# Kernel optimization log

Measured on AMD Instinct MI355X. Metric: run time of the kernel, lower is better.

Reference implementation:

```python
import jax, jax.numpy as jnp
import numpy as np

B, C, N, K, H = 8, 64, 4096, 32, 4
D = C // H  # head dim = 16
EPS = 1e-5  # BatchNorm eps (torch default)


def setup_inputs() -> dict:
    key = jax.random.key(0)
    ks = jax.random.split(key, 7)
    s = 0.05
    return {
        "x": jax.random.normal(ks[0], (B, C, N), jnp.float32),
        "wq": jax.random.normal(ks[1], (C, C), jnp.float32) * s,
        "wk": jax.random.normal(ks[2], (C, C), jnp.float32) * s,
        "wv": jax.random.normal(ks[3], (C, C), jnp.float32) * s,
        "w1": jax.random.normal(ks[4], (4 * C, C), jnp.float32) * s,
        "w2": jax.random.normal(ks[5], (C, 4 * C), jnp.float32) * s,
        "g1": jnp.ones((C,), jnp.float32),
        "b1": jnp.zeros((C,), jnp.float32),
        "g2": jnp.ones((C,), jnp.float32),
        "b2": jnp.zeros((C,), jnp.float32),
    }


def _bn(f, g, b):
    # BatchNorm1d in training mode: stats over (batch, points) per channel.
    # f: (B, N, C)
    mu = jnp.mean(f, axis=(0, 1))
    var = jnp.var(f, axis=(0, 1))  # biased, as torch uses for normalization
    return (f - mu) * jax.lax.rsqrt(var + EPS) * g + b


def reference(x, wq, wk, wv, w1, w2, g1, b1, g2, b2):
    feat = jnp.transpose(x, (0, 2, 1))  # (B, N, C)
    # KNN in feature space: negative squared distances, take top-K largest
    sq = jnp.sum(feat * feat, axis=-1)  # (B, N)
    neg_d = 2.0 * jnp.einsum('bnc,bmc->bnm', feat, feat) - sq[:, :, None] - sq[:, None, :]
    _, idx = jax.lax.top_k(neg_d, K)  # (B, N, K) int32
    # gather neighbors and form diffs
    nbrs = jax.vmap(lambda p, i: p[i])(feat, idx)  # (B, N, K, C)
    diff = nbrs - feat[:, :, None, :]
    # 1x1-conv projections (bias-free linear over channels)
    q = jnp.einsum('bnc,oc->bno', feat, wq).reshape(B, N, H, D)
    k = jnp.einsum('bnkc,oc->bnko', diff, wk).reshape(B, N, K, H, D)
    v = jnp.einsum('bnkc,oc->bnko', diff, wv).reshape(B, N, K, H, D)
    energy = jnp.einsum('bnhd,bnkhd->bnhk', q, k) / jnp.sqrt(jnp.float32(D))
    attn = jax.nn.softmax(energy, axis=-1)  # softmax over K neighbors
    out = jnp.einsum('bnhk,bnkhd->bnhd', attn, v).reshape(B, N, C)  # H-major merge
    f1 = _bn(feat + out, g1, b1)
    hid = jnp.einsum('bnc,oc->bno', f1, w1)
    hid = jnp.where(hid > 0, hid, 0.2 * hid)  # LeakyReLU(0.2)
    ff = jnp.einsum('bno,co->bnc', hid, w2)
    f2 = _bn(f1 + ff, g2, b2)
    return jnp.transpose(f2, (0, 2, 1))  # (B, C, N)
```

## Files before the change

### kernel.cpp

```cpp
#include <hip/hip_runtime.h>

#define Bdim 8
#define Cdim 64
#define Ndim 4096
#define Kdim 32
#define ROWS (Bdim*Ndim)
#define BN_EPS 1e-5f

using f32x4  = __attribute__((ext_vector_type(4))) float;
using f16x8  = __attribute__((ext_vector_type(8))) _Float16;

__device__ __forceinline__ float dot4(float4 a, float4 b){
  return a.x*b.x + a.y*b.y + a.z*b.z + a.w*b.w;
}
__device__ __forceinline__ int wofs(int o, int g){ return o*64 + (((g ^ ((o>>2)&7)))<<2); }
__device__ __forceinline__ unsigned keyOf(float f){
  unsigned u = __float_as_uint(f);
  return (u & 0x80000000u) ? ~u : (u ^ 0x80000000u);
}

__global__ __launch_bounds__(256) void prep_proj_kernel(const float* __restrict__ x,
    const float* __restrict__ wq, const float* __restrict__ wk,
    const float* __restrict__ wv,
    float* __restrict__ sq,
    float* __restrict__ Qo, float* __restrict__ PKo, float* __restrict__ PVo,
    float* __restrict__ accZ,
    float* __restrict__ featT, unsigned short* __restrict__ xh)
{
  __shared__ __align__(16) float ftile[64*68];
  __shared__ __align__(16) float Ws[3][64*64];
  const int tid = threadIdx.x;
  const int blk = blockIdx.x;
  const int b  = blk & 7;
  const int n0 = (blk >> 3) * 64;
  const size_t rowBase = (size_t)b*Ndim + n0;
  if (blk == 0) accZ[tid] = 0.f;
  for (int k=0;k<16;++k){
    int idx = tid + (k<<8);
    int c = idx>>6, nn = idx&63;
    ftile[nn*68+c] = x[((size_t)b*64+c)*Ndim + n0 + nn];
  }
  {
    const float* wp[3] = {wq, wk, wv};
    for (int m=0;m<3;++m)
      for (int k=0;k<16;++k){
        int idx = tid + (k<<8);
        int o = idx>>6, c = idx&63;
        Ws[m][wofs(o, c>>2) + (c&3)] = wp[m][o*64 + c];
      }
  }
  __syncthreads();
  for (int k=0;k<16;++k){
    int idx = tid + (k<<8);
    int r = idx>>6, c = idx&63;
    float v = ftile[r*68+c];
    size_t o = (rowBase + r)*64 + c;
    featT[o] = v;
    _Float16 hh = (_Float16)v;
    xh[o] = *reinterpret_cast<unsigned short*>(&hh);
  }
  if (tid < 64){
    float a = 0.f;
    #pragma unroll
    for (int c=0;c<64;++c){ float v = ftile[tid*68+c]; a += v*v; }
    sq[b*Ndim + n0 + tid] = a;
  }
  const int tr = tid>>4, to = tid&15;
  float* outp[3] = {Qo, PKo, PVo};
  for (int m=0;m<3;++m){
    float acc[4][4];
    #pragma unroll
    for (int r=0;r<4;++r){ acc[r][0]=0.f; acc[r][1]=0.f; acc[r][2]=0.f; acc[r][3]=0.f; }
    #pragma unroll 4
    for (int c4=0;c4<16;++c4){
      float4 f[4], w[4];
      #pragma unroll
      for (int r=0;r<4;++r)  f[r] = *(const float4*)&ftile[(4*tr+r)*68 + (c4<<2)];
      #pragma unroll
      for (int oo=0;oo<4;++oo) w[oo] = *(const float4*)&Ws[m][wofs(4*to+oo, c4)];
      #pragma unroll
      for (int r=0;r<4;++r)
        #pragma unroll
        for (int oo=0;oo<4;++oo)
          acc[r][oo] += dot4(f[r], w[oo]);
    }
    #pragma unroll
    for (int r=0;r<4;++r){
      float4 v; v.x=acc[r][0]; v.y=acc[r][1]; v.z=acc[r][2]; v.w=acc[r][3];
      *(float4*)&outp[m][(rowBase + 4*tr + r)*64 + 4*to] = v;
    }
  }
}

__global__ __launch_bounds__(1024) void knn_attn_kernel(
    const float* __restrict__ sq,
    const float* __restrict__ Qm, const float* __restrict__ PKm, const float* __restrict__ PVm,
    const float* __restrict__ featT, const unsigned short* __restrict__ xh,
    float* __restrict__ t1, float* __restrict__ bn1s, float* __restrict__ bn1q)
{
  __shared__ __align__(16) unsigned char smem[43328];
  float* fnS  = (float*)smem;
  float* qvS  = (float*)(smem + 4096);
  float* pknS = (float*)(smem + 8192);
  float* pvnS = (float*)(smem + 12288);
  unsigned short* dbuf = (unsigned short*)(smem + 16384);
  int*   candI  = (int*)(smem + 16384);
  float* red1   = (float*)(smem + 20480);
  float* red2   = (float*)(smem + 24576);
  float* enS    = (float*)(smem + 33024);
  int*   outIdx = (int*)(smem + 41216);
  float* sqnS   = (float*)(smem + 43264);

  const int tid  = threadIdx.x;
  const int lane = tid & 63;
  const int w    = tid >> 6;
  const int blk  = blockIdx.x;
  const int b    = blk & 7;
  const int n0   = (blk >> 3) << 4;
  const size_t b4096 = (size_t)b << 12;

  {
    int j = tid>>6, c = tid&63;
    size_t ro = (b4096 + n0 + j)*64 + c;
    fnS[tid]  = featT[ro];
    qvS[tid]  = Qm[ro];
    pknS[tid] = PKm[ro];
    pvnS[tid] = PVm[ro];
    if (tid < 16) sqnS[tid] = sq[b4096 + n0 + tid];
    if (tid < 512) outIdx[tid] = n0 + (tid>>5);
  }
  __syncthreads();

  const unsigned short* xhb = xh + (b4096 << 6);
  const float* sqb = sq + b4096;
  const int l15  = lane & 15;
  const int acol = (lane >> 4) << 3;
  const int qrow = (lane >> 4) << 2;

  unsigned kk[32];

  {
    f16x8 a0 = *(const f16x8*)&xhb[(size_t)(n0 + l15)*64 + acol];
    f16x8 a1 = *(const f16x8*)&xhb[(size_t)(n0 + l15)*64 + acol + 32];
    #pragma unroll
    for (int ch=0; ch<16; ++ch){
      unsigned short* bw = dbuf + (ch&1)*(16*260);
      const int brow = (ch<<8) + (w<<4) + l15;
      f16x8 b0 = *(const f16x8*)&xhb[(size_t)brow*64 + acol];
      f16x8 b1 = *(const f16x8*)&xhb[(size_t)brow*64 + acol + 32];
      f32x4 acc = {0.f,0.f,0.f,0.f};
      acc = __builtin_amdgcn_mfma_f32_16x16x32_f16(a0, b0, acc, 0, 0, 0);
      acc = __builtin_amdgcn_mfma_f32_16x16x32_f16(a1, b1, acc, 0, 0, 0);
      float sm = sqb[brow];
      #pragma unroll
      for (int r=0;r<4;++r){
        float v = fmaf(2.f, acc[r], -sm);
        int k16 = (int)fmaf(v, 128.f, 40960.f);
        k16 = k16 < 0 ? 0 : (k16 > 65535 ? 65535 : k16);
        bw[(qrow+r)*260 + (w<<4) + l15] = (unsigned short)k16;
      }
      __syncthreads();
      unsigned k01 = *(const unsigned*)&bw[w*260 + (lane<<2)];
      unsigned k23 = *(const unsigned*)&bw[w*260 + (lane<<2) + 2];
      kk[(ch<<1)]   = k01;
      kk[(ch<<1)+1] = k23;
    }
  }

  const unsigned long long below = (1ull<<lane) - 1ull;
  int sQ;
  {
    unsigned mE = 0, mO = 0;
    #pragma unroll
    for (int i=0;i<16;++i){
      unsigned u = kk[i];
      unsigned hv = u >> 16, lv = u & 0xFFFFu;
      unsigned m = hv > lv ? hv : lv;
      mE = mE > m ? mE : m;
    }
    #pragma unroll
    for (int i=16;i<32;++i){
      unsigned u = kk[i];
      unsigned hv = u >> 16, lv = u & 0xFFFFu;
      unsigned m = hv > lv ? hv : lv;
      mO = mO > m ? mO : m;
    }
    unsigned T = 0;
    #pragma unroll
    for (int bit=15; bit>=0; --bit){
      unsigned cand = T | (1u<<bit);
      int c2 = (int)__popcll(__ballot(mE >= cand)) + (int)__popcll(__ballot(mO >= cand));
      if (c2 >= 32) T = cand;
    }
    const unsigned Tm = (T > 16u) ? (T - 16u) : 0u;
    int base = 0;
    #pragma unroll
    for (int j=0;j<64;++j){
      unsigned word = kk[((j>>2)<<1) | ((j>>1)&1)];
      unsigned key  = (j&1) ? (word>>16) : (word & 0xFFFFu);
      bool isc = (key >= Tm);
      unsigned long long mk = __ballot(isc);
      if (isc){
        int slot = base + (int)__popcll(mk & below);
        if (slot < 64) candI[(w<<6)+slot] = ((j>>2)<<8) + (lane<<2) + (j&3);
      }
      base += (int)__popcll(mk);
    }
    if (base > 64){
      base = 0;
      #pragma unroll
      for (int j=0;j<64;++j){
        unsigned word = kk[((j>>2)<<1) | ((j>>1)&1)];
        unsigned key  = (j&1) ? (word>>16) : (word & 0xFFFFu);
        bool isc = (key >= T);
        unsigned long long mk = __ballot(isc);
        if (isc){
          int slot = base + (int)__popcll(mk & below);
          if (slot < 64) candI[(w<<6)+slot] = ((j>>2)<<8) + (lane<<2) + (j&3);
        }
        base += (int)__popcll(mk);
      }
    }
    sQ = base < 64 ? base : 64;
  }

  {
    int mj = -1; unsigned keyE = 0u;
    if (lane < sQ){
      mj = candI[(w<<6)+lane];
      const float* fm = featT + (b4096 + mj)*64;
      const float* fq = fnS + (w<<6);
      float as = 0.f;
      #pragma unroll 4
      for (int d4=0; d4<16; ++d4){
        float4 qv = *(const float4*)&fq[d4<<2];
        float4 mv = *(const float4*)&fm[d4<<2];
        as = fmaf(qv.x, mv.x, as); as = fmaf(qv.y, mv.y, as);
        as = fmaf(qv.z, mv.z, as); as = fmaf(qv.w, mv.w, as);
      }
      float de = (2.f*as - sqnS[w]) - sq[b4096 + mj];
      keyE = keyOf(de);
    }
    unsigned long long C = ((unsigned long long)keyE << 32) |
                           (unsigned long long)(~(unsigned)mj);
    #pragma unroll
    for (int k2=2; k2<=64; k2<<=1){
      #pragma unroll
      for (int j2=k2>>1; j2>=1; j2>>=1){
        unsigned long long P = (unsigned long long)__shfl_xor((long long)C, j2, 64);
        bool lowIdx  = ((lane & j2) == 0);
        bool keepMax = (lowIdx == ((lane & k2) == 0));
        unsigned long long mx = C > P ? C : P;
        unsigned long long mn = C > P ? P : C;
        C = keepMax ? mx : mn;
      }
    }
    if (lane < 32) outIdx[(w<<5)+lane] = (int)(~(unsigned)(C & 0xFFFFFFFFull)) & (Ndim-1);
  }
  __syncthreads();

  #pragma unroll
  for (int p=0;p<2;++p){
    int task = tid + (p<<10);
    int jn = task>>7, h = (task>>5)&3, k2 = task&31;
    int mj = outIdx[(jn<<5)+k2] & (Ndim-1);
    const float4* pk4 = (const float4*)(PKm + (b4096 + mj)*64 + (h<<4));
    const float4* qq4 = (const float4*)&qvS[(jn<<6)+(h<<4)];
    const float4* nn4 = (const float4*)&pknS[(jn<<6)+(h<<4)];
    float e = 0.f;
    #pragma unroll
    for (int d=0;d<4;++d){
      float4 kv = pk4[d], qq = qq4[d], nn = nn4[d];
      e += qq.x*(kv.x-nn.x) + qq.y*(kv.y-nn.y) + qq.z*(kv.z-nn.z) + qq.w*(kv.w-nn.w);
    }
    enS[(jn<<7)+(h<<5)+k2] = e * 0.25f;
  }
  __syncthreads();

  {
    int g = tid>>4, l16 = tid&15;
    int jn = g>>2, h = g&3;
    float* ep = &enS[(jn<<7)+(h<<5)];
    float v0 = ep[l16], v1 = ep[l16+16];
    float mx = fmaxf(v0, v1);
    mx = fmaxf(mx, __shfl_xor(mx, 1, 64));
    mx = fmaxf(mx, __shfl_xor(mx, 2, 64));
    mx = fmaxf(mx, __shfl_xor(mx, 4, 64));
    mx = fmaxf(mx, __shfl_xor(mx, 8, 64));
    v0 = expf(v0-mx); v1 = expf(v1-mx);
    float s = v0+v1;
    s += __shfl_xor(s, 1, 64);
    s += __shfl_xor(s, 2, 64);
    s += __shfl_xor(s, 4, 64);
    s += __shfl_xor(s, 8, 64);
    float inv = 1.f/s;
    ep[l16] = v0*inv; ep[l16+16] = v1*inv;
  }
  __syncthreads();

  float tv;
  {
    int c = lane, h = c>>4;
    float a2 = 0.f;
    #pragma unroll 4
    for (int k2=0;k2<32;++k2){
      int mj = outIdx[(w<<5)+k2] & (Ndim-1);
      a2 += enS[(w<<7)+(h<<5)+k2] * (PVm[(b4096 + mj)*64 + c] - pvnS[(w<<6)+c]);
    }
    tv = fnS[(w<<6)+c] + a2;
    t1[(b4096 + n0 + w)*64 + c] = tv;
  }
  red1[tid] = tv;
  red2[tid] = tv*tv;
  __syncthreads();
  if (tid < 64){
    float S = 0.f, S2 = 0.f;
    #pragma unroll
    for (int j=0;j<16;++j){ S += red1[(j<<6)+tid]; S2 += red2[(j<<6)+tid]; }
    atomicAdd(&bn1s[tid], S);
    atomicAdd(&bn1q[tid], S2);
  }
}

__global__ __launch_bounds__(256) void mlp_kernel(const float* __restrict__ t1,
    const float* __restrict__ w1, const float* __restrict__ w2,
    const float* __restrict__ g1, const float* __restrict__ b1,
    const float* __restrict__ bns, const float* __restrict__ bnq,
    float* __restrict__ t2, float* __restrict__ bn2s, float* __restrict__ bn2q)
{
  __shared__ __align__(16) float f1l[64*68];
  __shared__ __align__(16) float hl[64*68];
  __shared__ __align__(16) float w1s[64*64];
  __shared__ __align__(16) float w2s[64*64];
  __shared__ float mu[64], rs[64], gg[64], bb[64];
  const int tid = threadIdx.x;
  if (tid < 64){
    float m = bns[tid] * (1.f/32768.f);
    float v = bnq[tid] * (1.f/32768.f) - m*m;
    mu[tid] = m; rs[tid] = 1.f/sqrtf(v + BN_EPS);
    gg[tid] = g1[tid]; bb[tid] = b1[tid];
  }
  __syncthreads();
  const size_t rowBase = (size_t)blockIdx.x*64;
  for (int k=0;k<16;++k){
    int idx = tid + (k<<8);
    int r = idx>>6, c = idx&63;
    float v = t1[(rowBase + r)*64 + c];
    f1l[r*68+c] = (v - mu[c])*rs[c]*gg[c] + bb[c];
  }
  const int tr = tid>>4, to = tid&15;
  float ff[4][4];
  #pragma unroll
  for (int r=0;r<4;++r){ ff[r][0]=0.f; ff[r][1]=0.f; ff[r][2]=0.f; ff[r][3]=0.f; }

  for (int hc=0; hc<4; ++hc){
    __syncthreads();
    for (int k=0;k<16;++k){
      int idx = tid + (k<<8);
      int o = idx>>6, c = idx&63;
      w1s[wofs(o, c>>2) + (c&3)] = w1[(size_t)(hc*64+o)*64 + c];
      w2s[wofs(o, c>>2) + (c&3)] = w2[(size_t)o*256 + hc*64 + c];
    }
    __syncthreads();
    float hv[4][4];
    #pragma unroll
    for (int r=0;r<4;++r){ hv[r][0]=0.f; hv[r][1]=0.f; hv[r][2]=0.f; hv[r][3]=0.f; }
    #pragma unroll 4
    for (int c4=0;c4<16;++c4){
      float4 f[4], w[4];
      #pragma unroll
      for (int r=0;r<4;++r)  f[r] = *(const float4*)&f1l[(4*tr+r)*68 + (c4<<2)];
      #pragma unroll
      for (int oo=0;oo<4;++oo) w[oo] = *(const float4*)&w1s[wofs(4*to+oo, c4)];
      #pragma unroll
      for (int r=0;r<4;++r)
        #pragma unroll
        for (int oo=0;oo<4;++oo)
          hv[r][oo] += dot4(f[r], w[oo]);
    }
    #pragma unroll
    for (int r=0;r<4;++r){
      float4 v;
      float x0=hv[r][0], x1=hv[r][1], x2=hv[r][2], x3=hv[r][3];
      v.x = (x0>0.f)?x0:0.2f*x0; v.y = (x1>0.f)?x1:0.2f*x1;
      v.z = (x2>0.f)?x2:0.2f*x2; v.w = (x3>0.f)?x3:0.2f*x3;
      *(float4*)&hl[(4*tr+r)*68 + 4*to] = v;
    }
    __syncthreads();
    #pragma unroll 4
    for (int o4=0;o4<16;++o4){
      float4 h[4], w[4];
      #pragma unroll
      for (int r=0;r<4;++r)  h[r] = *(const float4*)&hl[(4*tr+r)*68 + (o4<<2)];
      #pragma unroll
      for (int oo=0;oo<4;++oo) w[oo] = *(const float4*)&w2s[wofs(4*to+oo, o4)];
      #pragma unroll
      for (int r=0;r<4;++r)
        #pragma unroll
        for (int oo=0;oo<4;++oo)
          ff[r][oo] += dot4(h[r], w[oo]);
    }
  }
  float ls[4]  = {0.f,0.f,0.f,0.f};
  float ls2[4] = {0.f,0.f,0.f,0.f};
  #pragma unroll
  for (int r=0;r<4;++r){
    float4 v;
    v.x = f1l[(4*tr+r)*68 + 4*to+0] + ff[r][0];
    v.y = f1l[(4*tr+r)*68 + 4*to+1] + ff[r][1];
    v.z = f1l[(4*tr+r)*68 + 4*to+2] + ff[r][2];
    v.w = f1l[(4*tr+r)*68 + 4*to+3] + ff[r][3];
    *(float4*)&t2[(rowBase + 4*tr + r)*64 + 4*to] = v;
    ls[0]+=v.x; ls[1]+=v.y; ls[2]+=v.z; ls[3]+=v.w;
    ls2[0]+=v.x*v.x; ls2[1]+=v.y*v.y; ls2[2]+=v.z*v.z; ls2[3]+=v.w*v.w;
  }
  __syncthreads();
  #pragma unroll
  for (int i=0;i<4;++i){
    hl[tr*64 + 4*to + i]        = ls[i];
    hl[1024 + tr*64 + 4*to + i] = ls2[i];
  }
  __syncthreads();
  if (tid < 64){
    float S = 0.f, S2 = 0.f;
    #pragma unroll
    for (int g2=0; g2<16; ++g2){ S += hl[g2*64 + tid]; S2 += hl[1024 + g2*64 + tid]; }
    atomicAdd(&bn2s[tid], S);
    atomicAdd(&bn2q[tid], S2);
  }
}

__global__ __launch_bounds__(256) void final_kernel(const float* __restrict__ t2,
    const float* __restrict__ bns, const float* __restrict__ bnq,
    const float* __restrict__ g2, const float* __restrict__ b2,
    float* __restrict__ out)
{
  __shared__ float tile[64*65];
  __shared__ float mu[64], rs[64], gg[64], bb[64];
  const int tid = threadIdx.x;
  const int b = blockIdx.y;
  const int n0 = blockIdx.x*64;
  if (tid < 64){
    float m = bns[tid] * (1.f/32768.f);
    float v = bnq[tid] * (1.f/32768.f) - m*m;
    mu[tid] = m; rs[tid] = 1.f/sqrtf(v + BN_EPS);
    gg[tid] = g2[tid]; bb[tid] = b2[tid];
  }
  __syncthreads();
  for (int k=0;k<16;++k){
    int idx = tid + (k<<8);
    int r = idx>>6, c = idx&63;
    float v = t2[((size_t)b*Ndim + n0 + r)*64 + c];
    tile[r*65+c] = (v - mu[c])*rs[c]*gg[c] + bb[c];
  }
  __syncthreads();
  for (int k=0;k<16;++k){
    int idx = tid + (k<<8);
    int c = idx>>6, nn = idx&63;
    out[((size_t)b*64 + c)*Ndim + n0 + nn] = tile[nn*65+c];
  }
}

extern "C" void kernel_launch(void* const* d_in, const int* in_sizes, int n_in,
                              void* d_out, int out_size, void* d_ws, size_t ws_size,
                              hipStream_t stream)
{
  (void)in_sizes; (void)n_in; (void)out_size; (void)ws_size;
  const float* x  = (const float*)d_in[0];
  const float* wq = (const float*)d_in[1];
  const float* wk = (const float*)d_in[2];
  const float* wv = (const float*)d_in[3];
  const float* w1 = (const float*)d_in[4];
  const float* w2 = (const float*)d_in[5];
  const float* g1 = (const float*)d_in[6];
  const float* b1 = (const float*)d_in[7];
  const float* g2 = (const float*)d_in[8];
  const float* b2 = (const float*)d_in[9];
  float* out = (float*)d_out;

  const size_t NE = (size_t)ROWS*64;
  float* sq   = (float*)d_ws;
  float* Qb   = sq + ROWS;
  float* PKb  = Qb + NE;
  float* PVb  = PKb + NE;
  float* t1   = PVb + NE;
  float* t2   = t1 + NE;
  float* acc  = t2 + NE;
  unsigned short* xh = (unsigned short*)(acc + 256);

  prep_proj_kernel<<<dim3(512), 256, 0, stream>>>(x, wq, wk, wv, sq, Qb, PKb, PVb, acc, t2, xh);
  knn_attn_kernel<<<dim3(2048), 1024, 0, stream>>>(sq, Qb, PKb, PVb, t2, xh, t1, acc, acc+64);
  mlp_kernel<<<dim3(512), 256, 0, stream>>>(t1, w1, w2, g1, b1, acc, acc+64, t2, acc+128, acc+192);
  final_kernel<<<dim3(64,8), 256, 0, stream>>>(t2, acc+128, acc+192, g2, b2, out);
}
```

Before: 378.3 us.

## Prefetch next KNN chunk rows and fuse per-wave energy softmax without block barriers

The KNN distance loop now loads the next chunk's fp16 rows and squared norms one iteration ahead, so global load latency overlaps the MFMA and key-packing work. The attention energy and softmax stage is reorganised so each wave computes its own point's 4 heads x 32 neighbours in registers, with softmax done by 32-lane shuffles. This removes two block-wide barriers and the shared-memory round trip between energy and softmax. A barrier is added after the KNN loop, and prefetching costs extra registers.

```diff
diff --git a/kernel.cpp b/kernel.cpp
--- a/kernel.cpp
+++ b/kernel.cpp
@@ -142,16 +142,23 @@
   {
     f16x8 a0 = *(const f16x8*)&xhb[(size_t)(n0 + l15)*64 + acol];
     f16x8 a1 = *(const f16x8*)&xhb[(size_t)(n0 + l15)*64 + acol + 32];
+    int brow = (w<<4) + l15;
+    f16x8 b0 = *(const f16x8*)&xhb[(size_t)brow*64 + acol];
+    f16x8 b1 = *(const f16x8*)&xhb[(size_t)brow*64 + acol + 32];
+    float sm = sqb[brow];
     #pragma unroll
     for (int ch=0; ch<16; ++ch){
       unsigned short* bw = dbuf + (ch&1)*(16*260);
-      const int brow = (ch<<8) + (w<<4) + l15;
-      f16x8 b0 = *(const f16x8*)&xhb[(size_t)brow*64 + acol];
-      f16x8 b1 = *(const f16x8*)&xhb[(size_t)brow*64 + acol + 32];
       f32x4 acc = {0.f,0.f,0.f,0.f};
       acc = __builtin_amdgcn_mfma_f32_16x16x32_f16(a0, b0, acc, 0, 0, 0);
       acc = __builtin_amdgcn_mfma_f32_16x16x32_f16(a1, b1, acc, 0, 0, 0);
-      float sm = sqb[brow];
+      f16x8 nb0, nb1; float nsm = 0.f;
+      if (ch < 15){
+        const int nrow = ((ch+1)<<8) + (w<<4) + l15;
+        nb0 = *(const f16x8*)&xhb[(size_t)nrow*64 + acol];
+        nb1 = *(const f16x8*)&xhb[(size_t)nrow*64 + acol + 32];
+        nsm = sqb[nrow];
+      }
       #pragma unroll
       for (int r=0;r<4;++r){
         float v = fmaf(2.f, acc[r], -sm);
@@ -164,8 +171,10 @@
       unsigned k23 = *(const unsigned*)&bw[w*260 + (lane<<2) + 2];
       kk[(ch<<1)]   = k01;
       kk[(ch<<1)+1] = k23;
-    }
-  }
+      if (ch < 15){ b0 = nb0; b1 = nb1; sm = nsm; }
+    }
+  }
+  __syncthreads();
 
   const unsigned long long below = (1ull<<lane) - 1ull;
   int sQ;
@@ -257,46 +266,44 @@
     }
     if (lane < 32) outIdx[(w<<5)+lane] = (int)(~(unsigned)(C & 0xFFFFFFFFull)) & (Ndim-1);
   }
-  __syncthreads();
-
-  #pragma unroll
-  for (int p=0;p<2;++p){
-    int task = tid + (p<<10);
-    int jn = task>>7, h = (task>>5)&3, k2 = task&31;
-    int mj = outIdx[(jn<<5)+k2] & (Ndim-1);
-    const float4* pk4 = (const float4*)(PKm + (b4096 + mj)*64 + (h<<4));
-    const float4* qq4 = (const float4*)&qvS[(jn<<6)+(h<<4)];
-    const float4* nn4 = (const float4*)&pknS[(jn<<6)+(h<<4)];
-    float e = 0.f;
-    #pragma unroll
-    for (int d=0;d<4;++d){
-      float4 kv = pk4[d], qq = qq4[d], nn = nn4[d];
-      e += qq.x*(kv.x-nn.x) + qq.y*(kv.y-nn.y) + qq.z*(kv.z-nn.z) + qq.w*(kv.w-nn.w);
-    }
-    enS[(jn<<7)+(h<<5)+k2] = e * 0.25f;
-  }
-  __syncthreads();
-
-  {
-    int g = tid>>4, l16 = tid&15;
-    int jn = g>>2, h = g&3;
-    float* ep = &enS[(jn<<7)+(h<<5)];
-    float v0 = ep[l16], v1 = ep[l16+16];
-    float mx = fmaxf(v0, v1);
-    mx = fmaxf(mx, __shfl_xor(mx, 1, 64));
-    mx = fmaxf(mx, __shfl_xor(mx, 2, 64));
-    mx = fmaxf(mx, __shfl_xor(mx, 4, 64));
-    mx = fmaxf(mx, __shfl_xor(mx, 8, 64));
-    v0 = expf(v0-mx); v1 = expf(v1-mx);
-    float s = v0+v1;
-    s += __shfl_xor(s, 1, 64);
-    s += __shfl_xor(s, 2, 64);
-    s += __shfl_xor(s, 4, 64);
-    s += __shfl_xor(s, 8, 64);
-    float inv = 1.f/s;
-    ep[l16] = v0*inv; ep[l16+16] = v1*inv;
-  }
-  __syncthreads();
+
+  {
+    float at[2];
+    #pragma unroll
+    for (int p=0;p<2;++p){
+      int h  = (p<<1) | (lane>>5);
+      int k2 = lane & 31;
+      int mj = outIdx[(w<<5)+k2] & (Ndim-1);
+      const float4* pk4 = (const float4*)(PKm + (b4096 + mj)*64 + (h<<4));
+      const float4* qq4 = (const float4*)&qvS[(w<<6)+(h<<4)];
+      const float4* nn4 = (const float4*)&pknS[(w<<6)+(h<<4)];
+      float e = 0.f;
+      #pragma unroll
+      for (int d=0;d<4;++d){
+        float4 kv = pk4[d], qq = qq4[d], nn = nn4[d];
+        e += qq.x*(kv.x-nn.x) + qq.y*(kv.y-nn.y) + qq.z*(kv.z-nn.z) + qq.w*(kv.w-nn.w);
+      }
+      at[p] = e * 0.25f;
+    }
+    #pragma unroll
+    for (int p=0;p<2;++p){
+      float mx = at[p];
+      mx = fmaxf(mx, __shfl_xor(mx, 1, 64));
+      mx = fmaxf(mx, __shfl_xor(mx, 2, 64));
+      mx = fmaxf(mx, __shfl_xor(mx, 4, 64));
+      mx = fmaxf(mx, __shfl_xor(mx, 8, 64));
+      mx = fmaxf(mx, __shfl_xor(mx, 16, 64));
+      float ex = expf(at[p]-mx);
+      float s = ex;
+      s += __shfl_xor(s, 1, 64);
+      s += __shfl_xor(s, 2, 64);
+      s += __shfl_xor(s, 4, 64);
+      s += __shfl_xor(s, 8, 64);
+      s += __shfl_xor(s, 16, 64);
+      int h = (p<<1) | (lane>>5);
+      enS[(w<<7)+(h<<5)+(lane&31)] = ex / s;
+    }
+  }
 
   float tv;
   {
```

Result: slower. 416.3 us (+10.1%).
